# Kernel optimization log

Measured on AMD Instinct MI355X. Metric: run time of the kernel, lower is better.

Reference implementation:

```python
import jax, jax.numpy as jnp
import numpy as np

C = 10  # cluster_num
EMB = 64

def setup_inputs() -> dict:
    key = jax.random.key(0)
    ks = jax.random.split(key, 12)
    B, N, D = 8, 4096, 1024
    n_classes = 1
    data = jax.random.normal(ks[0], (B, N, D), dtype=jnp.float32)
    labels = jax.random.randint(ks[1], (B, N), 0, C, dtype=jnp.int32)
    s = 0.02
    return {
        "data": data,
        "labels": labels,
        # embedding_net: Conv2d(1024,64,1) == linear on feature dim
        "W1": jax.random.normal(ks[2], (EMB, D), dtype=jnp.float32) * s,
        "b1": jnp.zeros((EMB,), dtype=jnp.float32),
        # attention MLP: Linear(64,32) -> tanh -> Linear(32,1)
        "Wa1": jax.random.normal(ks[3], (32, EMB), dtype=jnp.float32) * s,
        "ba1": jnp.zeros((32,), dtype=jnp.float32),
        "Wa2": jax.random.normal(ks[4], (1, 32), dtype=jnp.float32) * s,
        "ba2": jnp.zeros((1,), dtype=jnp.float32),
        # fc6: Linear(64,32) -> ReLU -> (Dropout eval=identity) -> Linear(32,n_classes)
        "Wf1": jax.random.normal(ks[5], (32, EMB), dtype=jnp.float32) * s,
        "bf1": jnp.zeros((32,), dtype=jnp.float32),
        "Wf2": jax.random.normal(ks[6], (n_classes, 32), dtype=jnp.float32) * s,
        "bf2": jnp.zeros((n_classes,), dtype=jnp.float32),
    }

def _masked_softmax(x, mask):
    # faithful to the module's numeric trick
    x_masked = x * mask + (1.0 - 1.0 / (mask + 1e-5))
    x_max = jnp.max(x_masked, axis=1, keepdims=True)
    x_exp = jnp.exp(x - x_max) * mask
    return x_exp / jnp.sum(x_exp, axis=1, keepdims=True)

def reference(data, labels, W1, b1, Wa1, ba1, Wa2, ba2, Wf1, bf1, Wf2, bf2):
    B, N, D = data.shape
    # per-patch 1x1-conv embed + ReLU: [B,N,64]
    e = jax.nn.relu(jnp.einsum('bnd,ed->bne', data, W1) + b1)
    # ragged per-cluster mean (AdaptiveAvgPool over each cluster's patches)
    seg = (labels.astype(jnp.int32) + jnp.arange(B, dtype=jnp.int32)[:, None] * C).reshape(-1)
    sums = jax.ops.segment_sum(e.reshape(B * N, EMB), seg, num_segments=B * C)
    counts = jax.ops.segment_sum(jnp.ones((B * N,), dtype=jnp.float32), seg, num_segments=B * C)
    sums = sums.reshape(B, C, EMB)
    counts = counts.reshape(B, C)
    mask = (counts > 0).astype(jnp.float32)
    h = sums / jnp.maximum(counts, 1.0)[..., None]  # [B,C,64]
    # attention scores over clusters
    a = jnp.einsum('bce,oe->bco', jnp.tanh(jnp.einsum('bce,he->bch', h, Wa1) + ba1), Wa2) + ba2
    A = _masked_softmax(a[..., 0], mask)  # [B,C]
    M = jnp.einsum('bc,bce->be', A, h)    # [B,64]
    # fc6 (dropout is identity at inference)
    logits = jax.nn.relu(M @ Wf1.T + bf1) @ Wf2.T + bf2
    return logits
```

## Files before the change

kernel.cpp:

```cpp
#include <hip/hip_runtime.h>
#include <stdint.h>

#define NC 10
#define EMB 64
#define DD 1024
#define NP 4096
#define NB 8
#define BP 32
#define NBLK (NB * NP / BP)
#define PPB (NP / BP)
#define KCH 128
#define NCHUNK (DD / KCH)
#define WFRAG_U32 65536

typedef __attribute__((ext_vector_type(4))) float f32x4;
typedef __attribute__((ext_vector_type(8))) short short8;

union FragU {
    uint32_t u[4];
    int4     i;
    short8   s;
};

__global__ __launch_bounds__(256) void prep_wfrag(
    const float* __restrict__ W1, uint32_t* __restrict__ wf)
{
    const int tid  = blockIdx.x * 256 + threadIdx.x;
    const int lane = tid & 63;
    const int hl   = (tid >> 6) & 1;
    const int ct   = (tid >> 7) & 3;
    const int kg   = tid >> 9;
    const int e    = ct * 16 + (lane & 15);
    const int k0   = kg * 32 + (lane >> 4) * 8;
    const float* src = W1 + (size_t)e * DD + k0;

    uint32_t out[4];
#pragma unroll
    for (int q = 0; q < 4; ++q) {
        float x0 = src[2 * q], x1 = src[2 * q + 1];
        uint32_t b0 = __float_as_uint(x0), b1 = __float_as_uint(x1);
        uint32_t h0 = (b0 + 0x7fffu + ((b0 >> 16) & 1u)) >> 16;
        uint32_t h1 = (b1 + 0x7fffu + ((b1 >> 16) & 1u)) >> 16;
        if (hl == 0) {
            out[q] = h0 | (h1 << 16);
        } else {
            float r0 = x0 - __uint_as_float(h0 << 16);
            float r1 = x1 - __uint_as_float(h1 << 16);
            uint32_t c0 = __float_as_uint(r0), c1 = __float_as_uint(r1);
            uint32_t l0 = (c0 + 0x7fffu + ((c0 >> 16) & 1u)) >> 16;
            uint32_t l1 = (c1 + 0x7fffu + ((c1 >> 16) & 1u)) >> 16;
            out[q] = l0 | (l1 << 16);
        }
    }
    *(uint4*)(wf + (size_t)tid * 4) = make_uint4(out[0], out[1], out[2], out[3]);
}

__global__ __launch_bounds__(512, 8) void embed_mfma(
    const float* __restrict__ data, const int* __restrict__ labels,
    const uint32_t* __restrict__ wf, const float* __restrict__ b1,
    float* __restrict__ psum, float* __restrict__ pcnt, int use_atomic)
{
    __shared__ float csum[NC][EMB];
    __shared__ float ccnt[NC];
    __shared__ int   labs[BP];

    const int t    = threadIdx.x;
    const int lane = t & 63;
    const int w    = t >> 6;
    const int pt   = w >> 2;
    const int ct   = w & 3;
    const int bid  = blockIdx.x;
    const int bag  = bid >> 7;
    const int p0   = (bid & 127) * BP;

    for (int i = t; i < NC * EMB; i += 512) (&csum[0][0])[i] = 0.f;
    if (t < NC) ccnt[t] = 0.f;
    if (t < BP) labs[t] = labels[bag * NP + p0 + t];
    __syncthreads();

    const float* Ap = data + (size_t)(bag * NP + p0 + pt * 16 + (lane & 15)) * DD
                    + ((lane >> 4) << 3);
    const uint4* Wp = (const uint4*)wf + (size_t)(ct * 128 + lane);

    f32x4 acc = {};

#define PACK_HI(x0, x1) ((__float_as_uint(x1) & 0xffff0000u) | (__float_as_uint(x0) >> 16))

    for (int c = 0; c < NCHUNK; ++c) {
        float4 a[8];
        uint4  bw[8];
#pragma unroll
        for (int ks = 0; ks < 4; ++ks) {
            a[2 * ks]     = *(const float4*)(Ap + c * KCH + ks * 32);
            a[2 * ks + 1] = *(const float4*)(Ap + c * KCH + ks * 32 + 4);
        }
#pragma unroll
        for (int ks = 0; ks < 4; ++ks) {
            bw[2 * ks]     = Wp[(size_t)((c * 4 + ks) * 512)];
            bw[2 * ks + 1] = Wp[(size_t)((c * 4 + ks) * 512 + 64)];
        }
#pragma unroll
        for (int ks = 0; ks < 4; ++ks) {
            const float4 a0 = a[2 * ks], a1 = a[2 * ks + 1];
            FragU ahi, alo;
            ahi.u[0] = PACK_HI(a0.x, a0.y);
            ahi.u[1] = PACK_HI(a0.z, a0.w);
            ahi.u[2] = PACK_HI(a1.x, a1.y);
            ahi.u[3] = PACK_HI(a1.z, a1.w);
            float r0 = a0.x - __uint_as_float(__float_as_uint(a0.x) & 0xffff0000u);
            float r1 = a0.y - __uint_as_float(__float_as_uint(a0.y) & 0xffff0000u);
            float r2 = a0.z - __uint_as_float(__float_as_uint(a0.z) & 0xffff0000u);
            float r3 = a0.w - __uint_as_float(__float_as_uint(a0.w) & 0xffff0000u);
            float r4 = a1.x - __uint_as_float(__float_as_uint(a1.x) & 0xffff0000u);
            float r5 = a1.y - __uint_as_float(__float_as_uint(a1.y) & 0xffff0000u);
            float r6 = a1.z - __uint_as_float(__float_as_uint(a1.z) & 0xffff0000u);
            float r7 = a1.w - __uint_as_float(__float_as_uint(a1.w) & 0xffff0000u);
            alo.u[0] = PACK_HI(r0, r1);
            alo.u[1] = PACK_HI(r2, r3);
            alo.u[2] = PACK_HI(r4, r5);
            alo.u[3] = PACK_HI(r6, r7);
            FragU bhi, blo;
            bhi.i = *(const int4*)&bw[2 * ks];
            blo.i = *(const int4*)&bw[2 * ks + 1];
            acc = __builtin_amdgcn_mfma_f32_16x16x32_bf16(ahi.s, bhi.s, acc, 0, 0, 0);
            acc = __builtin_amdgcn_mfma_f32_16x16x32_bf16(ahi.s, blo.s, acc, 0, 0, 0);
            acc = __builtin_amdgcn_mfma_f32_16x16x32_bf16(alo.s, bhi.s, acc, 0, 0, 0);
        }
    }

    {
        const int emb = ct * 16 + (lane & 15);
        const float bb = b1[emb];
#pragma unroll
        for (int r = 0; r < 4; ++r) {
            const int patch = pt * 16 + (lane >> 4) * 4 + r;
            float v = fmaxf(acc[r] + bb, 0.f);
            atomicAdd(&csum[labs[patch]][emb], v);
        }
    }
    if (t < BP) atomicAdd(&ccnt[labs[t]], 1.0f);
    __syncthreads();

    if (use_atomic) {
        for (int i = t; i < NC * EMB; i += 512)
            atomicAdd(&psum[(size_t)bag * NC * EMB + i], (&csum[0][0])[i]);
        if (t < NC) atomicAdd(&pcnt[bag * NC + t], ccnt[t]);
    } else {
        for (int i = t; i < NC * EMB; i += 512)
            psum[(size_t)bid * NC * EMB + i] = (&csum[0][0])[i];
        if (t < NC) pcnt[bid * NC + t] = ccnt[t];
    }
}

__global__ __launch_bounds__(256) void head_kernel(
    const float* __restrict__ psum, const float* __restrict__ pcnt, int npb,
    const float* __restrict__ Wa1, const float* __restrict__ ba1,
    const float* __restrict__ Wa2, const float* __restrict__ ba2,
    const float* __restrict__ Wf1, const float* __restrict__ bf1,
    const float* __restrict__ Wf2, const float* __restrict__ bf2,
    float* __restrict__ out)
{
    __shared__ float h[NC][EMB];
    __shared__ float cnt_s[NC];
    __shared__ float mask[NC];
    __shared__ float att[NC][32];
    __shared__ float a_s[NC];
    __shared__ float A_s[NC];
    __shared__ float M_s[EMB];
    __shared__ float f_s[32];

    const int b = blockIdx.x;
    const int t = threadIdx.x;

    if (t < NC) {
        float s = 0.f;
        for (int pb = 0; pb < npb; ++pb) s += pcnt[(size_t)(b * npb + pb) * NC + t];
        cnt_s[t] = s;
        mask[t]  = s > 0.f ? 1.f : 0.f;
    }
    __syncthreads();
    for (int i = t; i < NC * EMB; i += 256) {
        float s = 0.f;
#pragma unroll 8
        for (int pb = 0; pb < npb; ++pb) s += psum[(size_t)(b * npb + pb) * NC * EMB + i];
        (&h[0][0])[i] = s / fmaxf(cnt_s[i >> 6], 1.f);
    }
    __syncthreads();

    for (int task = t; task < NC * 32; task += 256) {
        int c = task >> 5, hh = task & 31;
        float s = ba1[hh];
        for (int e = 0; e < EMB; ++e) s = fmaf(Wa1[hh * EMB + e], h[c][e], s);
        att[c][hh] = tanhf(s);
    }
    __syncthreads();

    if (t < NC) {
        float s = ba2[0];
        for (int hh = 0; hh < 32; ++hh) s = fmaf(Wa2[hh], att[t][hh], s);
        a_s[t] = s;
    }
    __syncthreads();

    if (t == 0) {
        float xmax = -1e30f;
        for (int c = 0; c < NC; ++c) {
            float xm = a_s[c] * mask[c] + (1.0f - 1.0f / (mask[c] + 1e-5f));
            xmax = fmaxf(xmax, xm);
        }
        float ex[NC], ssum = 0.f;
        for (int c = 0; c < NC; ++c) {
            ex[c] = expf(a_s[c] - xmax) * mask[c];
            ssum += ex[c];
        }
        for (int c = 0; c < NC; ++c) A_s[c] = ex[c] / ssum;
    }
    __syncthreads();

    if (t < EMB) {
        float s = 0.f;
        for (int c = 0; c < NC; ++c) s = fmaf(A_s[c], h[c][t], s);
        M_s[t] = s;
    }
    __syncthreads();

    if (t < 32) {
        float s = bf1[t];
        for (int e = 0; e < EMB; ++e) s = fmaf(Wf1[t * EMB + e], M_s[e], s);
        f_s[t] = fmaxf(s, 0.f);
    }
    __syncthreads();

    if (t == 0) {
        float s = bf2[0];
        for (int hh = 0; hh < 32; ++hh) s = fmaf(Wf2[hh], f_s[hh], s);
        out[b] = s;
    }
}

extern "C" void kernel_launch(void* const* d_in, const int* in_sizes, int n_in,
                              void* d_out, int out_size, void* d_ws, size_t ws_size,
                              hipStream_t stream)
{
    const float* data   = (const float*)d_in[0];
    const int*   labels = (const int*)  d_in[1];
    const float* W1     = (const float*)d_in[2];
    const float* b1     = (const float*)d_in[3];
    const float* Wa1    = (const float*)d_in[4];
    const float* ba1    = (const float*)d_in[5];
    const float* Wa2    = (const float*)d_in[6];
    const float* ba2    = (const float*)d_in[7];
    const float* Wf1    = (const float*)d_in[8];
    const float* bf1    = (const float*)d_in[9];
    const float* Wf2    = (const float*)d_in[10];
    const float* bf2    = (const float*)d_in[11];

    uint32_t* wfrag = (uint32_t*)d_ws;
    float* psum = (float*)(wfrag + WFRAG_U32);

    prep_wfrag<<<64, 256, 0, stream>>>(W1, wfrag);

    const size_t need_na = (size_t)WFRAG_U32 * 4 +
                           ((size_t)NBLK * NC * EMB + (size_t)NBLK * NC) * sizeof(float);
    if (ws_size >= need_na) {
        float* pcnt = psum + (size_t)NBLK * NC * EMB;
        embed_mfma<<<NBLK, 512, 0, stream>>>(data, labels, wfrag, b1, psum, pcnt, 0);
        head_kernel<<<NB, 256, 0, stream>>>(psum, pcnt, PPB, Wa1, ba1, Wa2, ba2,
                                            Wf1, bf1, Wf2, bf2, (float*)d_out);
    } else {
        float* pcnt = psum + (size_t)NB * NC * EMB;
        hipMemsetAsync((void*)psum, 0,
                       (size_t)(NB * NC * EMB + NB * NC) * sizeof(float), stream);
        embed_mfma<<<NBLK, 512, 0, stream>>>(data, labels, wfrag, b1, psum, pcnt, 1);
        head_kernel<<<NB, 256, 0, stream>>>(psum, pcnt, 1, Wa1, ba1, Wa2, ba2,
                                            Wf1, bf1, Wf2, bf2, (float*)d_out);
    }
}
```

Baseline: 295.2 us.

## Stage A and W tiles in LDS via async global_load_lds with double buffering

The embed kernel now copies the data and weight-fragment tiles straight from global memory into LDS with global_load_lds, double-buffered across 32 K-chunks of 32 elements, with an XOR swizzle on the A tile. Blocks shrink to 256 threads and each wave computes two patch tiles against one 16-column slice, so B fragments are reused. This is meant to overlap the memory-bound data stream with the MFMA work and cut register pressure. In exchange it adds a __syncthreads per chunk and smaller per-chunk transfers, which may limit how much memory traffic is in flight.

```diff
diff --git a/kernel.cpp b/kernel.cpp
--- a/kernel.cpp
+++ b/kernel.cpp
@@ -9,18 +9,19 @@
 #define BP 32
 #define NBLK (NB * NP / BP)
 #define PPB (NP / BP)
-#define KCH 128
-#define NCHUNK (DD / KCH)
+#define NCHUNK 32
 #define WFRAG_U32 65536
 
 typedef __attribute__((ext_vector_type(4))) float f32x4;
 typedef __attribute__((ext_vector_type(8))) short short8;
 
-union FragU {
-    uint32_t u[4];
-    int4     i;
-    short8   s;
-};
+union FragU { uint32_t u[4]; int4 i; short8 s; };
+
+__device__ __forceinline__ void gld_lds16(const void* g, void* l) {
+    __builtin_amdgcn_global_load_lds(
+        (const __attribute__((address_space(1))) void*)g,
+        (__attribute__((address_space(3))) void*)l, 16, 0, 0);
+}
 
 __global__ __launch_bounds__(256) void prep_wfrag(
     const float* __restrict__ W1, uint32_t* __restrict__ wf)
@@ -55,11 +56,13 @@
     *(uint4*)(wf + (size_t)tid * 4) = make_uint4(out[0], out[1], out[2], out[3]);
 }
 
-__global__ __launch_bounds__(512, 8) void embed_mfma(
+__global__ __launch_bounds__(256, 4) void embed_mfma(
     const float* __restrict__ data, const int* __restrict__ labels,
     const uint32_t* __restrict__ wf, const float* __restrict__ b1,
     float* __restrict__ psum, float* __restrict__ pcnt, int use_atomic)
 {
+    __shared__ char  AsB[2][4096];
+    __shared__ uint4 Wl[2][512];
     __shared__ float csum[NC][EMB];
     __shared__ float ccnt[NC];
     __shared__ int   labs[BP];
@@ -67,41 +70,53 @@
     const int t    = threadIdx.x;
     const int lane = t & 63;
     const int w    = t >> 6;
-    const int pt   = w >> 2;
-    const int ct   = w & 3;
     const int bid  = blockIdx.x;
     const int bag  = bid >> 7;
-    const int p0   = (bid & 127) * BP;
-
-    for (int i = t; i < NC * EMB; i += 512) (&csum[0][0])[i] = 0.f;
+    const int p0   = (bid & 127) << 5;
+
+    for (int i = t; i < NC * EMB; i += 256) (&csum[0][0])[i] = 0.f;
     if (t < NC) ccnt[t] = 0.f;
     if (t < BP) labs[t] = labels[bag * NP + p0 + t];
-    __syncthreads();
-
-    const float* Ap = data + (size_t)(bag * NP + p0 + pt * 16 + (lane & 15)) * DD
-                    + ((lane >> 4) << 3);
-    const uint4* Wp = (const uint4*)wf + (size_t)(ct * 128 + lane);
-
-    f32x4 acc = {};
+
+    const char* Abase = (const char*)data + (size_t)(bag * NP + p0) * 4096;
+    const uint4* wf4  = (const uint4*)wf;
+
+    const int      arow = (w << 3) + (lane >> 3);
+    const unsigned acol = (unsigned)(((lane & 7) << 4) ^ ((lane >> 3) << 4));
+    const char* Asrc = Abase + (size_t)arow * 4096 + acol;
+    char* Adst[2] = { (char*)&AsB[0][0] + (w << 10), (char*)&AsB[1][0] + (w << 10) };
+    const uint4* Wsrc = wf4 + (w << 6) + lane;
+    char* Wdst[2] = { (char*)&Wl[0][0] + (w << 10), (char*)&Wl[1][0] + (w << 10) };
+
+    gld_lds16(Asrc, Adst[0]);
+    gld_lds16(Wsrc, Wdst[0]);
+    gld_lds16(Wsrc + 256, Wdst[0] + 4096);
+    __syncthreads();
+
+    f32x4 acc[2] = {};
+    const unsigned sw   = (unsigned)((lane & 7) << 4);
+    const unsigned cb0  = (unsigned)((lane >> 4) << 5);
+    const unsigned alo_ = cb0 ^ sw;
+    const unsigned row0 = ((unsigned)(lane & 15)) << 7;
 
 #define PACK_HI(x0, x1) ((__float_as_uint(x1) & 0xffff0000u) | (__float_as_uint(x0) >> 16))
 
     for (int c = 0; c < NCHUNK; ++c) {
-        float4 a[8];
-        uint4  bw[8];
-#pragma unroll
-        for (int ks = 0; ks < 4; ++ks) {
-            a[2 * ks]     = *(const float4*)(Ap + c * KCH + ks * 32);
-            a[2 * ks + 1] = *(const float4*)(Ap + c * KCH + ks * 32 + 4);
-        }
-#pragma unroll
-        for (int ks = 0; ks < 4; ++ks) {
-            bw[2 * ks]     = Wp[(size_t)((c * 4 + ks) * 512)];
-            bw[2 * ks + 1] = Wp[(size_t)((c * 4 + ks) * 512 + 64)];
-        }
-#pragma unroll
-        for (int ks = 0; ks < 4; ++ks) {
-            const float4 a0 = a[2 * ks], a1 = a[2 * ks + 1];
+        const int buf = c & 1;
+        const char* asb = &AsB[buf][0];
+        if (c + 1 < NCHUNK) {
+            gld_lds16(Asrc + (c + 1) * 128, Adst[buf ^ 1]);
+            const uint4* ws = Wsrc + (size_t)(c + 1) * 512;
+            gld_lds16(ws, Wdst[buf ^ 1]);
+            gld_lds16(ws + 256, Wdst[buf ^ 1] + 4096);
+        }
+        FragU bhi, blo;
+        bhi.i = *(const int4*)&Wl[buf][(w << 7) + lane];
+        blo.i = *(const int4*)&Wl[buf][(w << 7) + 64 + lane];
+#pragma unroll
+        for (int pt = 0; pt < 2; ++pt) {
+            const float4 a0 = *(const float4*)(asb + (pt << 11) + row0 + alo_);
+            const float4 a1 = *(const float4*)(asb + (pt << 11) + row0 + (alo_ ^ 16u));
             FragU ahi, alo;
             ahi.u[0] = PACK_HI(a0.x, a0.y);
             ahi.u[1] = PACK_HI(a0.z, a0.w);
@@ -119,34 +134,34 @@
             alo.u[1] = PACK_HI(r2, r3);
             alo.u[2] = PACK_HI(r4, r5);
             alo.u[3] = PACK_HI(r6, r7);
-            FragU bhi, blo;
-            bhi.i = *(const int4*)&bw[2 * ks];
-            blo.i = *(const int4*)&bw[2 * ks + 1];
-            acc = __builtin_amdgcn_mfma_f32_16x16x32_bf16(ahi.s, bhi.s, acc, 0, 0, 0);
-            acc = __builtin_amdgcn_mfma_f32_16x16x32_bf16(ahi.s, blo.s, acc, 0, 0, 0);
-            acc = __builtin_amdgcn_mfma_f32_16x16x32_bf16(alo.s, bhi.s, acc, 0, 0, 0);
-        }
+            acc[pt] = __builtin_amdgcn_mfma_f32_16x16x32_bf16(ahi.s, bhi.s, acc[pt], 0, 0, 0);
+            acc[pt] = __builtin_amdgcn_mfma_f32_16x16x32_bf16(ahi.s, blo.s, acc[pt], 0, 0, 0);
+            acc[pt] = __builtin_amdgcn_mfma_f32_16x16x32_bf16(alo.s, bhi.s, acc[pt], 0, 0, 0);
+        }
+        __syncthreads();
     }
 
     {
-        const int emb = ct * 16 + (lane & 15);
+        const int emb = (w << 4) + (lane & 15);
         const float bb = b1[emb];
 #pragma unroll
-        for (int r = 0; r < 4; ++r) {
-            const int patch = pt * 16 + (lane >> 4) * 4 + r;
-            float v = fmaxf(acc[r] + bb, 0.f);
-            atomicAdd(&csum[labs[patch]][emb], v);
-        }
+        for (int pt = 0; pt < 2; ++pt)
+#pragma unroll
+            for (int r = 0; r < 4; ++r) {
+                const int patch = (pt << 4) + ((lane >> 4) << 2) + r;
+                float v = fmaxf(acc[pt][r] + bb, 0.f);
+                atomicAdd(&csum[labs[patch]][emb], v);
+            }
     }
     if (t < BP) atomicAdd(&ccnt[labs[t]], 1.0f);
     __syncthreads();
 
     if (use_atomic) {
-        for (int i = t; i < NC * EMB; i += 512)
+        for (int i = t; i < NC * EMB; i += 256)
             atomicAdd(&psum[(size_t)bag * NC * EMB + i], (&csum[0][0])[i]);
         if (t < NC) atomicAdd(&pcnt[bag * NC + t], ccnt[t]);
     } else {
-        for (int i = t; i < NC * EMB; i += 512)
+        for (int i = t; i < NC * EMB; i += 256)
             psum[(size_t)bid * NC * EMB + i] = (&csum[0][0])[i];
         if (t < NC) pcnt[bid * NC + t] = ccnt[t];
     }
@@ -264,14 +279,14 @@
                            ((size_t)NBLK * NC * EMB + (size_t)NBLK * NC) * sizeof(float);
     if (ws_size >= need_na) {
         float* pcnt = psum + (size_t)NBLK * NC * EMB;
-        embed_mfma<<<NBLK, 512, 0, stream>>>(data, labels, wfrag, b1, psum, pcnt, 0);
+        embed_mfma<<<NBLK, 256, 0, stream>>>(data, labels, wfrag, b1, psum, pcnt, 0);
         head_kernel<<<NB, 256, 0, stream>>>(psum, pcnt, PPB, Wa1, ba1, Wa2, ba2,
                                             Wf1, bf1, Wf2, bf2, (float*)d_out);
     } else {
         float* pcnt = psum + (size_t)NB * NC * EMB;
         hipMemsetAsync((void*)psum, 0,
                        (size_t)(NB * NC * EMB + NB * NC) * sizeof(float), stream);
-        embed_mfma<<<NBLK, 512, 0, stream>>>(data, labels, wfrag, b1, psum, pcnt, 1);
+        embed_mfma<<<NBLK, 256, 0, stream>>>(data, labels, wfrag, b1, psum, pcnt, 1);
         head_kernel<<<NB, 256, 0, stream>>>(psum, pcnt, 1, Wa1, ba1, Wa2, ba2,
                                             Wf1, bf1, Wf2, bf2, (float*)d_out);
     }
```

After: 274.7 us. 7.0% less time.
